# Kernel optimization log

Hardware: AMD Instinct MI355X
Metric: run time of the kernel (lower is better)

Reference implementation:

```python
import jax, jax.numpy as jnp
import numpy as np

D_MODEL = 2048
N_HEAD = 16
N_KV_HEAD = 4
D_HEAD = D_MODEL // N_HEAD  # 128
WINDOW = 512
B, T = 2, 2048


def _rope_tables(T, d_head, base=10000.0):
    inv = 1.0 / (base ** (np.arange(0, d_head, 2, dtype=np.float32) / d_head))
    t = np.arange(T, dtype=np.float32)
    freqs = np.outer(t, inv)  # [T, d_head//2]
    return jnp.asarray(np.cos(freqs)), jnp.asarray(np.sin(freqs))


def setup_inputs() -> dict:
    key = jax.random.key(0)
    ks = jax.random.split(key, 5)
    cos, sin = _rope_tables(T, D_HEAD)
    s = 1.0 / np.sqrt(D_MODEL)
    return {
        "x": jax.random.normal(ks[0], (B, T, D_MODEL), jnp.float32),
        "cos": cos,
        "sin": sin,
        "Wq": jax.random.normal(ks[1], (D_MODEL, D_MODEL), jnp.float32) * s,
        "Wk": jax.random.normal(ks[2], (D_MODEL, N_KV_HEAD * D_HEAD), jnp.float32) * s,
        "Wv": jax.random.normal(ks[3], (D_MODEL, N_KV_HEAD * D_HEAD), jnp.float32) * s,
        "Wo": jax.random.normal(ks[4], (D_MODEL, D_MODEL), jnp.float32) * s,
    }


def _apply_rope(t, cos, sin):
    # t: [B, T, H, D]; cos/sin: [T, D//2]; interleaved-pair (complex) rotation
    tr = t[..., 0::2]
    ti = t[..., 1::2]
    c = cos[None, :, None, :]
    s = sin[None, :, None, :]
    out_r = tr * c - ti * s
    out_i = tr * s + ti * c
    return jnp.stack([out_r, out_i], axis=-1).reshape(t.shape)


def reference(x, cos, sin, Wq, Wk, Wv, Wo):
    Bx, Tx, C = x.shape
    q = (x @ Wq).reshape(Bx, Tx, N_HEAD, D_HEAD)       # [B,T,H,D]
    k = (x @ Wk).reshape(Bx, Tx, N_KV_HEAD, D_HEAD)    # [B,T,Hkv,D]
    v = (x @ Wv).reshape(Bx, Tx, N_KV_HEAD, D_HEAD)
    q = _apply_rope(q, cos, sin)
    k = _apply_rope(k, cos, sin)
    n_rep = N_HEAD // N_KV_HEAD
    k = jnp.repeat(k, n_rep, axis=2)  # [B,T,H,D]
    v = jnp.repeat(v, n_rep, axis=2)
    scale = 1.0 / np.sqrt(D_HEAD)
    att = jnp.einsum("bihd,bjhd->bhij", q, k) * scale  # [B,H,T,T]
    i = jnp.arange(Tx)[:, None]
    j = jnp.arange(Tx)[None, :]
    mask = (j <= i) & (j >= i - WINDOW + 1)            # causal sliding window
    att = jnp.where(mask[None, None], att, -jnp.inf)
    att = jax.nn.softmax(att, axis=-1)
    y = jnp.einsum("bhij,bjhd->bihd", att, v).reshape(Bx, Tx, C)
    return y @ Wo
```

## Files before the change

kernel.cpp:

```cpp
#include <hip/hip_runtime.h>
#include <hip/hip_bf16.h>
#include <cstdint>
#include <cstddef>

#define B_ 2
#define T_ 2048
#define NH 16
#define NKV 4
#define DH 128
#define DM 2048
#define WIN 512

typedef __attribute__((ext_vector_type(4))) float f32x4;
typedef __attribute__((ext_vector_type(8))) __bf16 bf16x8;

using bf16 = __hip_bfloat16;

__device__ inline void gload_lds16(const void* g, void* l) {
  __builtin_amdgcn_global_load_lds(
      (const __attribute__((address_space(1))) void*)g,
      (__attribute__((address_space(3))) void*)l, 16, 0, 0);
}

__device__ inline unsigned pack_bf2(float a, float b) {
  unsigned short ua = __builtin_bit_cast(unsigned short, __float2bfloat16(a));
  unsigned short ub = __builtin_bit_cast(unsigned short, __float2bfloat16(b));
  return (unsigned)ua | ((unsigned)ub << 16);
}

#define FBAR()                           \
  do {                                   \
    asm volatile("" ::: "memory");       \
    __builtin_amdgcn_s_barrier();        \
    asm volatile("" ::: "memory");       \
  } while (0)

__global__ __launch_bounds__(256) void k_prep(const float* __restrict__ x,
                                              const float* __restrict__ Wq,
                                              const float* __restrict__ Wk,
                                              const float* __restrict__ Wv,
                                              const float* __restrict__ Wo,
                                              bf16* __restrict__ xb,
                                              bf16* __restrict__ Wqkvt,
                                              bf16* __restrict__ Wot) {
  int id = blockIdx.x;
  int tid = threadIdx.x;
  if (id >= 2560) {
    size_t base = (size_t)(id - 2560) * 4096 + tid * 16;
#pragma unroll
    for (int j = 0; j < 4; ++j) {
      float4 v = *(const float4*)(x + base + j * 4);
      ushort4 o;
      o.x = __builtin_bit_cast(unsigned short, __float2bfloat16(v.x));
      o.y = __builtin_bit_cast(unsigned short, __float2bfloat16(v.y));
      o.z = __builtin_bit_cast(unsigned short, __float2bfloat16(v.z));
      o.w = __builtin_bit_cast(unsigned short, __float2bfloat16(v.w));
      *(ushort4*)(xb + base + j * 4) = o;
    }
    return;
  }
  const float* W;
  bf16* Wt;
  int N, bx, by;
  if (id < 1024) { W = Wq; Wt = Wqkvt; N = 2048; bx = id & 31; by = id >> 5; }
  else if (id < 1280) { id -= 1024; W = Wk; Wt = Wqkvt + (size_t)2048 * 2048; N = 512; bx = id & 7; by = id >> 3; }
  else if (id < 1536) { id -= 1280; W = Wv; Wt = Wqkvt + (size_t)2560 * 2048; N = 512; bx = id & 7; by = id >> 3; }
  else { id -= 1536; W = Wo; Wt = Wot; N = 2048; bx = id & 31; by = id >> 5; }

  __shared__ float tile[64][65];
  int n0 = bx * 64, k0 = by * 64;
  int tx = tid & 63, tg = tid >> 6;
#pragma unroll
  for (int r = 0; r < 16; ++r) {
    int k = tg * 16 + r;
    tile[k][tx] = W[(size_t)(k0 + k) * N + n0 + tx];
  }
  __syncthreads();
#pragma unroll
  for (int r = 0; r < 16; ++r) {
    int nn = tg * 16 + r;
    Wt[(size_t)(n0 + nn) * 2048 + k0 + tx] = __float2bfloat16(tile[tx][nn]);
  }
}

template <int BN, bool OUT_BF16>
__global__ __launch_bounds__(512, 2) void k_gemm8(const bf16* __restrict__ A,
                                                  const bf16* __restrict__ Bt,
                                                  void* __restrict__ Cout,
                                                  int M, int N, int K) {
  constexpr int NR = BN / 64;
  constexpr int NH0 = (NR + 1) / 2;
  constexpr int NH1 = NR - NH0;
  constexpr int VMN = 2 + NH0;
  __shared__ __align__(16) char As_[2][32768];
  __shared__ __align__(16) char Bs_[2][BN * 128];

  const int tid = threadIdx.x;
  const int w = tid >> 6, lane = tid & 63;
  const int li = lane & 15, g = lane >> 4;
  const int wm = w >> 2, wn = w & 3;

  const int nwg = gridDim.x * gridDim.y;
  int bid = blockIdx.y * gridDim.x + blockIdx.x;
  bid = (bid & 7) * (nwg >> 3) + (bid >> 3);
  const int m0 = (bid / gridDim.x) * 256;
  const int n0 = (bid % gridDim.x) * BN;

  const int ntiles = K >> 6;
  const int NT2 = ntiles >> 1;

  auto sA = [&](int buf, int tile, int half, int issue) {
    if (tile >= ntiles) return;
    const int R0 = half * 64 + issue * 128;
    const int rr = R0 + w * 8 + (lane >> 3);
    const int sl = lane & 7;
    const bf16* src = A + (size_t)(m0 + rr) * K + tile * 64 + ((sl ^ (rr & 7)) * 8);
    gload_lds16(src, As_[buf] + (R0 + w * 8) * 128);
  };
  auto sB = [&](int buf, int tile, int half, int issue) {
    if (tile >= ntiles) return;
    const int slot = issue * 8 + w;
    const int per = (half ? NH1 : NH0) * 2;
    const int wng = slot / per, within = slot % per;
    const int block = wng * (NR * 2) + (half ? NH0 * 2 : 0) + within;
    const int rr = block * 8 + (lane >> 3);
    const int sl = lane & 7;
    const bf16* src = Bt + (size_t)(n0 + rr) * K + tile * 64 + ((sl ^ (rr & 7)) * 8);
    gload_lds16(src, Bs_[buf] + block * 1024);
  };
  auto sBh = [&](int buf, int tile, int half) {
    sB(buf, tile, half, 0);
    if ((half ? NH1 : NH0) == 2) sB(buf, tile, half, 1);
  };

  const int swz0 = (g ^ (li & 7)) * 16;
  const int swz1 = ((4 + g) ^ (li & 7)) * 16;
  bf16x8 af[8], b0v[NH0 * 2], b1v[NH1 * 2];
  f32x4 acc[8][NR] = {};

  auto readA = [&](int buf, int mh) {
#pragma unroll
    for (int m = 0; m < 4; ++m) {
      const char* p = As_[buf] + (wm * 128 + mh * 64 + m * 16 + li) * 128;
      af[m * 2 + 0] = *(const bf16x8*)(p + swz0);
      af[m * 2 + 1] = *(const bf16x8*)(p + swz1);
    }
  };
  auto readB0 = [&](int buf) {
#pragma unroll
    for (int n = 0; n < NH0; ++n) {
      const char* p = Bs_[buf] + (wn * (NR * 16) + n * 16 + li) * 128;
      b0v[n * 2 + 0] = *(const bf16x8*)(p + swz0);
      b0v[n * 2 + 1] = *(const bf16x8*)(p + swz1);
    }
  };
  auto readB1 = [&](int buf) {
#pragma unroll
    for (int n = 0; n < NH1; ++n) {
      const char* p = Bs_[buf] + (wn * (NR * 16) + NH0 * 16 + n * 16 + li) * 128;
      b1v[n * 2 + 0] = *(const bf16x8*)(p + swz0);
      b1v[n * 2 + 1] = *(const bf16x8*)(p + swz1);
    }
  };
  auto MMA0 = [&](int mh) {
    __builtin_amdgcn_s_setprio(1);
#pragma unroll
    for (int m = 0; m < 4; ++m)
#pragma unroll
      for (int n = 0; n < NH0; ++n)
#pragma unroll
        for (int kk = 0; kk < 2; ++kk)
          acc[mh * 4 + m][n] = __builtin_amdgcn_mfma_f32_16x16x32_bf16(
              af[m * 2 + kk], b0v[n * 2 + kk], acc[mh * 4 + m][n], 0, 0, 0);
    __builtin_amdgcn_s_setprio(0);
  };
  auto MMA1 = [&](int mh) {
    __builtin_amdgcn_s_setprio(1);
#pragma unroll
    for (int m = 0; m < 4; ++m)
#pragma unroll
      for (int n = 0; n < NH1; ++n)
#pragma unroll
        for (int kk = 0; kk < 2; ++kk)
          acc[mh * 4 + m][NH0 + n] = __builtin_amdgcn_mfma_f32_16x16x32_bf16(
              af[m * 2 + kk], b1v[n * 2 + kk], acc[mh * 4 + m][NH0 + n], 0, 0, 0);
    __builtin_amdgcn_s_setprio(0);
  };
  auto VMW = [&](bool last) {
    if (last) {
      asm volatile("s_waitcnt vmcnt(0)" ::: "memory");
    } else {
      if constexpr (VMN == 4)
        asm volatile("s_waitcnt vmcnt(4)" ::: "memory");
      else
        asm volatile("s_waitcnt vmcnt(3)" ::: "memory");
    }
    __builtin_amdgcn_sched_barrier(0);
  };

  sA(0, 0, 0, 0); sA(0, 0, 0, 1); sA(0, 0, 1, 0); sA(0, 0, 1, 1);
  sBh(0, 0, 0); sBh(0, 0, 1);
  sA(1, 1, 0, 0); sA(1, 1, 0, 1);
  sBh(1, 1, 0);
  if constexpr (VMN == 4)
    asm volatile("s_waitcnt vmcnt(4)" ::: "memory");
  else
    asm volatile("s_waitcnt vmcnt(3)" ::: "memory");
  __builtin_amdgcn_sched_barrier(0);
  FBAR();

  for (int itr = 0; itr < NT2; ++itr) {
    const int t = itr * 2;
    const bool last = (itr == NT2 - 1);
    readA(0, 0); readB0(0);
    sA(1, t + 1, 1, 0); sA(1, t + 1, 1, 1);
    FBAR(); MMA0(0); FBAR();
    readB1(0);
    sBh(1, t + 1, 1);
    FBAR(); MMA1(0); FBAR();
    readA(0, 1);
    sA(0, t + 2, 0, 0); sA(0, t + 2, 0, 1);
    FBAR(); MMA0(1); FBAR();
    sBh(0, t + 2, 0);
    VMW(last);
    FBAR(); MMA1(1); FBAR();
    readA(1, 0); readB0(1);
    sA(0, t + 2, 1, 0); sA(0, t + 2, 1, 1);
    FBAR(); MMA0(0); FBAR();
    readB1(1);
    sBh(0, t + 2, 1);
    FBAR(); MMA1(0); FBAR();
    readA(1, 1);
    sA(1, t + 3, 0, 0); sA(1, t + 3, 0, 1);
    FBAR(); MMA0(1); FBAR();
    sBh(1, t + 3, 0);
    VMW(last);
    FBAR(); MMA1(1); FBAR();
  }

#pragma unroll
  for (int mf = 0; mf < 8; ++mf)
#pragma unroll
    for (int nf = 0; nf < NR; ++nf)
#pragma unroll
      for (int r = 0; r < 4; ++r) {
        int row = m0 + wm * 128 + mf * 16 + g * 4 + r;
        int col = n0 + wn * (NR * 16) + nf * 16 + li;
        float v = acc[mf][nf][r];
        if constexpr (OUT_BF16)
          ((bf16*)Cout)[(size_t)row * N + col] = __float2bfloat16(v);
        else
          ((float*)Cout)[(size_t)row * N + col] = v;
      }
}

__global__ __launch_bounds__(256) void k_rope_vtrans(bf16* __restrict__ qkv,
                                                     const float* __restrict__ cosT,
                                                     const float* __restrict__ sinT,
                                                     bf16* __restrict__ vt) {
  int id = blockIdx.x;
  int tid = threadIdx.x;
  if (id < 20480) {
    int p = id * 256 + tid;
    int i = p & 63;
    int h20 = (p >> 6) % 20;
    int bt = p / (64 * 20);
    int t = bt & (T_ - 1);
    float c = cosT[t * 64 + i], s = sinT[t * 64 + i];
    bool isq = h20 < 16;
    int col = isq ? h20 * DH : DM + (h20 - 16) * DH;
    float sc = isq ? 0.08838834764831845f : 1.0f;
    size_t base = (size_t)bt * 3072 + col + 2 * i;
    float tr = __bfloat162float(qkv[base]);
    float ti = __bfloat162float(qkv[base + 1]);
    qkv[base] = __float2bfloat16((tr * c - ti * s) * sc);
    qkv[base + 1] = __float2bfloat16((tr * s + ti * c) * sc);
    return;
  }
  int v = id - 20480;
  __shared__ bf16 tile[64][72];
  int bt0 = (v & 63) * 64, c0 = (v >> 6) * 64;
  int tx = tid & 63, tg = tid >> 6;
#pragma unroll
  for (int r = 0; r < 16; ++r) {
    int row = tg * 16 + r;
    tile[row][tx] = qkv[(size_t)(bt0 + row) * 3072 + 2560 + c0 + tx];
  }
  __syncthreads();
#pragma unroll
  for (int r = 0; r < 16; ++r) {
    int row2 = tg * 16 + r;
    vt[(size_t)(c0 + row2) * (B_ * T_) + bt0 + tx] = tile[tx][row2];
  }
}

__global__ __launch_bounds__(512) void k_attn(const bf16* __restrict__ qkv,
                                              const bf16* __restrict__ vt,
                                              bf16* __restrict__ Y) {
  __shared__ __align__(16) char Ks[2][9216];
  __shared__ __align__(16) char Vs[2][10240];
  __shared__ __align__(16) char Pl[8][1280];
  const int lane = threadIdx.x & 63;
  const int w = threadIdx.x >> 6;
  const int li = lane & 15, g = lane >> 4;
  const int t0 = ((int)gridDim.x - 1 - (int)blockIdx.x) * 32;
  const int b = blockIdx.y / NKV, kvh = blockIdx.y % NKV;
  const int h = kvh * 4 + (w >> 1);
  const int qrow0 = t0 + (w & 1) * 16;
  const int t = qrow0 + li;

  bf16x8 qf[4];
  const bf16* qbase = qkv + (size_t)(b * T_ + qrow0 + li) * 3072 + h * DH;
#pragma unroll
  for (int dk = 0; dk < 4; ++dk) qf[dk] = *(const bf16x8*)(qbase + dk * 32 + g * 8);

  float mrow = -1e4f;
  float srow = 0.f;
  f32x4 acc[8] = {};

  int ks0 = t0 - (WIN - 1);
  if (ks0 < 0) ks0 = 0;
  ks0 &= ~31;
  const int nt = (t0 + 31 - ks0) / 32 + 1;

  const bf16* kgbase = qkv + (size_t)(b * T_) * 3072 + DM + kvh * DH;
  const bf16* vgbase = vt + (size_t)(kvh * DH) * (B_ * T_) + b * T_;

  auto STAGE = [&](int buf, int kt) {
    for (int c = w; c < 19; c += 8) {
      if (c < 9) {
        int slot = c * 64 + lane;
        int row = slot / 17, cc = slot % 17;
        if (slot >= 544) { row = 0; cc = 0; }
        if (cc == 16) cc = 0;
        const bf16* src = kgbase + (size_t)(kt + row) * 3072 + cc * 8;
        gload_lds16(src, Ks[buf] + c * 1024);
      } else {
        int c2 = c - 9;
        int slot = c2 * 64 + lane;
        int row = slot / 5, cc = slot % 5;
        if (cc == 4) cc = 0;
        const bf16* src = vgbase + (size_t)row * (B_ * T_) + kt + cc * 8;
        gload_lds16(src, Vs[buf] + c2 * 1024);
      }
    }
  };

  STAGE(0, ks0);
  __syncthreads();
  int cur = 0;

  for (int it = 0; it < nt; ++it) {
    const int kt = ks0 + it * 32;
    if (it + 1 < nt) STAGE(cur ^ 1, kt + 32);

    f32x4 sc[2] = {};
#pragma unroll
    for (int n = 0; n < 2; ++n)
#pragma unroll
      for (int dk = 0; dk < 4; ++dk) {
        bf16x8 kf = *(const bf16x8*)(Ks[cur] + (n * 16 + li) * 272 + dk * 64 + g * 16);
        sc[n] = __builtin_amdgcn_mfma_f32_16x16x32_bf16(kf, qf[dk], sc[n], 0, 0, 0);
      }

    float p[2][4];
    float pmax = -1e30f;
#pragma unroll
    for (int n = 0; n < 2; ++n)
#pragma unroll
      for (int r = 0; r < 4; ++r) {
        int key = kt + n * 16 + g * 4 + r;
        bool valid = (key <= t) && (key > t - WIN);
        float pv = valid ? sc[n][r] : -1e30f;
        p[n][r] = pv;
        pmax = fmaxf(pmax, pv);
      }
    pmax = fmaxf(pmax, __shfl_xor(pmax, 16));
    pmax = fmaxf(pmax, __shfl_xor(pmax, 32));

    float nm = fmaxf(mrow, pmax);
    float alpha = __expf(mrow - nm);
    mrow = nm;
    float rs = 0.f;
#pragma unroll
    for (int n = 0; n < 2; ++n)
#pragma unroll
      for (int r = 0; r < 4; ++r) {
        p[n][r] = __expf(p[n][r] - nm);
        rs += p[n][r];
      }
    rs += __shfl_xor(rs, 16);
    rs += __shfl_xor(rs, 32);
    srow = srow * alpha + rs;

#pragma unroll
    for (int n = 0; n < 2; ++n) {
      *(unsigned*)(Pl[w] + li * 80 + n * 32 + g * 8) = pack_bf2(p[n][0], p[n][1]);
      *(unsigned*)(Pl[w] + li * 80 + n * 32 + g * 8 + 4) = pack_bf2(p[n][2], p[n][3]);
    }

    float af_[4];
#pragma unroll
    for (int r = 0; r < 4; ++r) af_[r] = __shfl(alpha, (g << 2) + r);
#pragma unroll
    for (int db = 0; db < 8; ++db)
#pragma unroll
      for (int r = 0; r < 4; ++r) acc[db][r] *= af_[r];

    bf16x8 pf = *(const bf16x8*)(Pl[w] + li * 80 + g * 16);
#pragma unroll
    for (int db = 0; db < 8; ++db) {
      bf16x8 vf = *(const bf16x8*)(Vs[cur] + (db * 16 + li) * 80 + g * 16);
      acc[db] = __builtin_amdgcn_mfma_f32_16x16x32_bf16(pf, vf, acc[db], 0, 0, 0);
    }

    __syncthreads();
    cur ^= 1;
  }

  float inv[4];
#pragma unroll
  for (int r = 0; r < 4; ++r) inv[r] = 1.f / __shfl(srow, (g << 2) + r);
  bf16* ybase = Y + (size_t)(b * T_ + qrow0 + (g << 2)) * DM + h * DH;
#pragma unroll
  for (int r = 0; r < 4; ++r)
#pragma unroll
    for (int db = 0; db < 8; ++db)
      ybase[(size_t)r * DM + db * 16 + li] = __float2bfloat16(acc[db][r] * inv[r]);
}

extern "C" void kernel_launch(void* const* d_in, const int* in_sizes, int n_in,
                              void* d_out, int out_size, void* d_ws, size_t ws_size,
                              hipStream_t stream) {
  const float* x = (const float*)d_in[0];
  const float* cosT = (const float*)d_in[1];
  const float* sinT = (const float*)d_in[2];
  const float* Wq = (const float*)d_in[3];
  const float* Wk = (const float*)d_in[4];
  const float* Wv = (const float*)d_in[5];
  const float* Wo = (const float*)d_in[6];
  float* out = (float*)d_out;

  char* ws = (char*)d_ws;
  bf16* xb = (bf16*)ws;     ws += (size_t)4096 * 2048 * 2;
  bf16* Wqkvt = (bf16*)ws;  ws += (size_t)3072 * 2048 * 2;
  bf16* Wot = (bf16*)ws;    ws += (size_t)2048 * 2048 * 2;
  bf16* qkv = (bf16*)ws;    ws += (size_t)4096 * 3072 * 2;
  bf16* yb = xb;
  bf16* vt = Wqkvt;

  k_prep<<<4608, 256, 0, stream>>>(x, Wq, Wk, Wv, Wo, xb, Wqkvt, Wot);

  k_gemm8<192, true><<<dim3(3072 / 192, 4096 / 256), 512, 0, stream>>>(xb, Wqkvt, qkv, 4096, 3072, 2048);

  k_rope_vtrans<<<20992, 256, 0, stream>>>(qkv, cosT, sinT, vt);

  k_attn<<<dim3(T_ / 32, B_ * NKV), 512, 0, stream>>>(qkv, vt, yb);

  k_gemm8<128, false><<<dim3(2048 / 128, 4096 / 256), 512, 0, stream>>>(yb, Wot, out, 4096, 2048, 2048);
}
```

Measured before the change: 171.8 us.

## Fuse RoPE and V transpose into QKV GEMM epilogue; skip redundant softmax rescale

The QKV GEMM epilogue now applies RoPE and the q scale in registers, using a lane shuffle to fetch the pair partner, and writes V directly in transposed layout into a separate buffer. This removes the separate rope/vtrans kernel launch and its full read-modify-write pass over qkv, which is now narrowed to a 2560-column stride. In attention, the accumulator rescale is skipped when no row's running max changes across the wave. The epilogue gains scattered cos/sin loads and strided 8-byte V stores, and the rescale skip adds a wave vote on every iteration.

```diff
diff --git a/kernel.cpp b/kernel.cpp
--- a/kernel.cpp
+++ b/kernel.cpp
@@ -10,6 +10,7 @@
 #define DH 128
 #define DM 2048
 #define WIN 512
+#define QKS 2560
 
 typedef __attribute__((ext_vector_type(4))) float f32x4;
 typedef __attribute__((ext_vector_type(8))) __bf16 bf16x8;
@@ -83,11 +84,14 @@
   }
 }
 
-template <int BN, bool OUT_BF16>
+template <int BN, int EPI>
 __global__ __launch_bounds__(512, 2) void k_gemm8(const bf16* __restrict__ A,
                                                   const bf16* __restrict__ Bt,
                                                   void* __restrict__ Cout,
-                                                  int M, int N, int K) {
+                                                  int M, int N, int K,
+                                                  const float* __restrict__ cosT,
+                                                  const float* __restrict__ sinT,
+                                                  bf16* __restrict__ vt) {
   constexpr int NR = BN / 64;
   constexpr int NH0 = (NR + 1) / 2;
   constexpr int NH1 = NR - NH0;
@@ -241,57 +245,41 @@
 #pragma unroll
   for (int mf = 0; mf < 8; ++mf)
 #pragma unroll
-    for (int nf = 0; nf < NR; ++nf)
-#pragma unroll
-      for (int r = 0; r < 4; ++r) {
-        int row = m0 + wm * 128 + mf * 16 + g * 4 + r;
-        int col = n0 + wn * (NR * 16) + nf * 16 + li;
-        float v = acc[mf][nf][r];
-        if constexpr (OUT_BF16)
-          ((bf16*)Cout)[(size_t)row * N + col] = __float2bfloat16(v);
-        else
-          ((float*)Cout)[(size_t)row * N + col] = v;
+    for (int nf = 0; nf < NR; ++nf) {
+      const int colc = n0 + wn * (NR * 16) + nf * 16;
+      const int col = colc + li;
+      const int row0 = m0 + wm * 128 + mf * 16 + g * 4;
+      if constexpr (EPI == 2) {
+        if (colc < QKS) {
+          const float qs = (colc < 2048) ? 0.08838834764831845f : 1.0f;
+          const int i = (col & 127) >> 1;
+          const float sgn = (li & 1) ? 1.0f : -1.0f;
+#pragma unroll
+          for (int r = 0; r < 4; ++r) {
+            const int trow = (row0 + r) & (T_ - 1);
+            float v = acc[mf][nf][r];
+            float pv = __shfl_xor(v, 1);
+            float c = cosT[trow * 64 + i], s = sinT[trow * 64 + i];
+            float o = (v * c + pv * (sgn * s)) * qs;
+            ((bf16*)Cout)[(size_t)(row0 + r) * QKS + col] = __float2bfloat16(o);
+          }
+        } else {
+          unsigned lo = pack_bf2(acc[mf][nf][0], acc[mf][nf][1]);
+          unsigned hi = pack_bf2(acc[mf][nf][2], acc[mf][nf][3]);
+          uint2 pk = {lo, hi};
+          *(uint2*)(vt + (size_t)(col - QKS) * (B_ * T_) + row0) = pk;
+        }
+      } else {
+#pragma unroll
+        for (int r = 0; r < 4; ++r) {
+          float v = acc[mf][nf][r];
+          if constexpr (EPI == 1)
+            ((bf16*)Cout)[(size_t)(row0 + r) * N + col] = __float2bfloat16(v);
+          else
+            ((float*)Cout)[(size_t)(row0 + r) * N + col] = v;
+        }
       }
-}
-
-__global__ __launch_bounds__(256) void k_rope_vtrans(bf16* __restrict__ qkv,
-                                                     const float* __restrict__ cosT,
-                                                     const float* __restrict__ sinT,
-                                                     bf16* __restrict__ vt) {
-  int id = blockIdx.x;
-  int tid = threadIdx.x;
-  if (id < 20480) {
-    int p = id * 256 + tid;
-    int i = p & 63;
-    int h20 = (p >> 6) % 20;
-    int bt = p / (64 * 20);
-    int t = bt & (T_ - 1);
-    float c = cosT[t * 64 + i], s = sinT[t * 64 + i];
-    bool isq = h20 < 16;
-    int col = isq ? h20 * DH : DM + (h20 - 16) * DH;
-    float sc = isq ? 0.08838834764831845f : 1.0f;
-    size_t base = (size_t)bt * 3072 + col + 2 * i;
-    float tr = __bfloat162float(qkv[base]);
-    float ti = __bfloat162float(qkv[base + 1]);
-    qkv[base] = __float2bfloat16((tr * c - ti * s) * sc);
-    qkv[base + 1] = __float2bfloat16((tr * s + ti * c) * sc);
-    return;
-  }
-  int v = id - 20480;
-  __shared__ bf16 tile[64][72];
-  int bt0 = (v & 63) * 64, c0 = (v >> 6) * 64;
-  int tx = tid & 63, tg = tid >> 6;
-#pragma unroll
-  for (int r = 0; r < 16; ++r) {
-    int row = tg * 16 + r;
-    tile[row][tx] = qkv[(size_t)(bt0 + row) * 3072 + 2560 + c0 + tx];
-  }
-  __syncthreads();
-#pragma unroll
-  for (int r = 0; r < 16; ++r) {
-    int row2 = tg * 16 + r;
-    vt[(size_t)(c0 + row2) * (B_ * T_) + bt0 + tx] = tile[tx][row2];
-  }
+    }
 }
 
 __global__ __launch_bounds__(512) void k_attn(const bf16* __restrict__ qkv,
@@ -310,7 +298,7 @@
   const int t = qrow0 + li;
 
   bf16x8 qf[4];
-  const bf16* qbase = qkv + (size_t)(b * T_ + qrow0 + li) * 3072 + h * DH;
+  const bf16* qbase = qkv + (size_t)(b * T_ + qrow0 + li) * QKS + h * DH;
 #pragma unroll
   for (int dk = 0; dk < 4; ++dk) qf[dk] = *(const bf16x8*)(qbase + dk * 32 + g * 8);
 
@@ -323,7 +311,7 @@
   ks0 &= ~31;
   const int nt = (t0 + 31 - ks0) / 32 + 1;
 
-  const bf16* kgbase = qkv + (size_t)(b * T_) * 3072 + DM + kvh * DH;
+  const bf16* kgbase = qkv + (size_t)(b * T_) * QKS + DM + kvh * DH;
   const bf16* vgbase = vt + (size_t)(kvh * DH) * (B_ * T_) + b * T_;
 
   auto STAGE = [&](int buf, int kt) {
@@ -333,7 +321,7 @@
         int row = slot / 17, cc = slot % 17;
         if (slot >= 544) { row = 0; cc = 0; }
         if (cc == 16) cc = 0;
-        const bf16* src = kgbase + (size_t)(kt + row) * 3072 + cc * 8;
+        const bf16* src = kgbase + (size_t)(kt + row) * QKS + cc * 8;
         gload_lds16(src, Ks[buf] + c * 1024);
       } else {
         int c2 = c - 9;
@@ -378,34 +366,37 @@
     pmax = fmaxf(pmax, __shfl_xor(pmax, 16));
     pmax = fmaxf(pmax, __shfl_xor(pmax, 32));
 
-    float nm = fmaxf(mrow, pmax);
-    float alpha = __expf(mrow - nm);
-    mrow = nm;
+    if (!__all(pmax <= mrow)) {
+      float nm = fmaxf(mrow, pmax);
+      float alpha = __expf(mrow - nm);
+      mrow = nm;
+      srow *= alpha;
+      float af_[4];
+#pragma unroll
+      for (int r = 0; r < 4; ++r) af_[r] = __shfl(alpha, (g << 2) + r);
+#pragma unroll
+      for (int db = 0; db < 8; ++db)
+#pragma unroll
+        for (int r = 0; r < 4; ++r) acc[db][r] *= af_[r];
+    }
+
     float rs = 0.f;
 #pragma unroll
     for (int n = 0; n < 2; ++n)
 #pragma unroll
       for (int r = 0; r < 4; ++r) {
-        p[n][r] = __expf(p[n][r] - nm);
+        p[n][r] = __expf(p[n][r] - mrow);
         rs += p[n][r];
       }
     rs += __shfl_xor(rs, 16);
     rs += __shfl_xor(rs, 32);
-    srow = srow * alpha + rs;
+    srow += rs;
 
 #pragma unroll
     for (int n = 0; n < 2; ++n) {
       *(unsigned*)(Pl[w] + li * 80 + n * 32 + g * 8) = pack_bf2(p[n][0], p[n][1]);
       *(unsigned*)(Pl[w] + li * 80 + n * 32 + g * 8 + 4) = pack_bf2(p[n][2], p[n][3]);
     }
-
-    float af_[4];
-#pragma unroll
-    for (int r = 0; r < 4; ++r) af_[r] = __shfl(alpha, (g << 2) + r);
-#pragma unroll
-    for (int db = 0; db < 8; ++db)
-#pragma unroll
-      for (int r = 0; r < 4; ++r) acc[db][r] *= af_[r];
 
     bf16x8 pf = *(const bf16x8*)(Pl[w] + li * 80 + g * 16);
 #pragma unroll
@@ -445,17 +436,17 @@
   bf16* xb = (bf16*)ws;     ws += (size_t)4096 * 2048 * 2;
   bf16* Wqkvt = (bf16*)ws;  ws += (size_t)3072 * 2048 * 2;
   bf16* Wot = (bf16*)ws;    ws += (size_t)2048 * 2048 * 2;
-  bf16* qkv = (bf16*)ws;    ws += (size_t)4096 * 3072 * 2;
+  bf16* qkv = (bf16*)ws;    ws += (size_t)4096 * QKS * 2;
+  bf16* vt = (bf16*)ws;     ws += (size_t)512 * 4096 * 2;
   bf16* yb = xb;
-  bf16* vt = Wqkvt;
 
   k_prep<<<4608, 256, 0, stream>>>(x, Wq, Wk, Wv, Wo, xb, Wqkvt, Wot);
 
-  k_gemm8<192, true><<<dim3(3072 / 192, 4096 / 256), 512, 0, stream>>>(xb, Wqkvt, qkv, 4096, 3072, 2048);
-
-  k_rope_vtrans<<<20992, 256, 0, stream>>>(qkv, cosT, sinT, vt);
+  k_gemm8<192, 2><<<dim3(3072 / 192, 4096 / 256), 512, 0, stream>>>(
+      xb, Wqkvt, qkv, 4096, 3072, 2048, cosT, sinT, vt);
 
   k_attn<<<dim3(T_ / 32, B_ * NKV), 512, 0, stream>>>(qkv, vt, yb);
 
-  k_gemm8<128, false><<<dim3(2048 / 128, 4096 / 256), 512, 0, stream>>>(yb, Wot, out, 4096, 2048, 2048);
-}
+  k_gemm8<128, 0><<<dim3(2048 / 128, 4096 / 256), 512, 0, stream>>>(
+      yb, Wot, out, 4096, 2048, 2048, nullptr, nullptr, nullptr);
+}
```

New measurement: 164.7 us. 4.1% less time.
